# Performance work log

Hardware: AMD Instinct MI355X
Metric: run time of the kernel (lower is better)

Reference implementation:

```python
import jax, jax.numpy as jnp
import numpy as np

B, D, K = 131072, 64, 4096

def setup_inputs() -> dict:
    key = jax.random.key(0)
    k1, k2 = jax.random.split(key)
    z_e = jax.random.normal(k1, (B, D), dtype=jnp.float32)
    # nn.init.uniform_(-1/K, 1/K)
    codebook = jax.random.uniform(k2, (K, D), dtype=jnp.float32, minval=-1.0 / K, maxval=1.0 / K)
    return {"z_e": z_e, "codebook": codebook}

def reference(z_e, codebook):
    # squared-distance expansion: ||z||^2 + ||e||^2 - 2 z.e  -> (B, K)
    z2 = jnp.sum(z_e * z_e, axis=1, keepdims=True)          # (B, 1)
    e2 = jnp.sum(codebook * codebook, axis=1)[None, :]       # (1, K)
    ze = jnp.einsum('bd,kd->bk', z_e, codebook)              # (B, K)
    dist = z2 + e2 - 2.0 * ze
    codes = jnp.argmin(dist, axis=1)                         # (B,) int
    z_q = codebook[codes]                                    # (B, D) gather
    return (z_q, codes)
```

## Files before the change

### kernel.cpp

```cpp
#include <hip/hip_runtime.h>
#include <math.h>
#include <stdint.h>

#define Bn 131072
#define Dn 64
#define Kn 4096
#define TK 64
#define NKT (Kn / TK)
#define TPR 4
#define NRD (NKT / TPR)

typedef _Float16 f16x8 __attribute__((ext_vector_type(8)));
typedef float f32x4 __attribute__((ext_vector_type(4)));

__device__ __forceinline__ unsigned umn(unsigned a, unsigned b) { return a < b ? a : b; }
__device__ __forceinline__ unsigned umed3(unsigned a, unsigned b, unsigned c) {
  unsigned d;
  asm("v_med3_u32 %0, %1, %2, %3" : "=v"(d) : "v"(a), "v"(b), "v"(c));
  return d;
}

__device__ __forceinline__ void stage16(const void* g, void* l) {
  __builtin_amdgcn_global_load_lds((const __attribute__((address_space(1))) unsigned int*)g,
                                   (__attribute__((address_space(3))) unsigned int*)l,
                                   16, 0, 0);
}

__global__ __launch_bounds__(256) void cvt_cb(const float* __restrict__ cb,
                                              unsigned char* __restrict__ img) {
  int u = blockIdx.x * 256 + threadIdx.x;
  int g = u >> 3;
  int p = u & 7;
  int kt = g >> 6;
  int n = g & 63;
  const float4* s = (const float4*)(cb + (size_t)g * Dn + p * 8);
  float4 c0 = s[0], c1 = s[1];
  f16x8 h;
  h[0] = (_Float16)(c0.x * 4096.f); h[1] = (_Float16)(c0.y * 4096.f);
  h[2] = (_Float16)(c0.z * 4096.f); h[3] = (_Float16)(c0.w * 4096.f);
  h[4] = (_Float16)(c1.x * 4096.f); h[5] = (_Float16)(c1.y * 4096.f);
  h[6] = (_Float16)(c1.z * 4096.f); h[7] = (_Float16)(c1.w * 4096.f);
  *(f16x8*)(img + (size_t)kt * 8192 + n * 128 + ((p ^ (n & 7)) << 4)) = h;
}

template <int RB, int WB>
__device__ __forceinline__ void round_body(int rd, int tid,
                                           unsigned char* smem_,
                                           const unsigned char* b0,
                                           const unsigned char* b1,
                                           const unsigned char* wsrc,
                                           const f16x8 (&A)[4][2],
                                           unsigned (&k1)[4][4], unsigned (&k2)[4][4],
                                           unsigned (&tg)[4], const f32x4 c256) {
  asm volatile("s_waitcnt vmcnt(0)" ::: "memory");
  __builtin_amdgcn_s_barrier();
  __builtin_amdgcn_sched_barrier(0);
  if (rd + 1 < NRD) {
#pragma unroll
    for (int j = 0; j < TPR; ++j) {
      const unsigned char* gs = wsrc + ((size_t)(rd + 1) * TPR + j) * 8192;
      stage16(gs, smem_ + WB + j * 8192 + tid * 16);
      stage16(gs + 4096, smem_ + WB + j * 8192 + 4096 + tid * 16);
    }
  }
#pragma unroll
  for (int j = 0; j < TPR; ++j) {
#pragma unroll
    for (int t = 0; t < 4; ++t) {
      const f16x8 B0 = *(const f16x8*)(b0 + RB + j * 8192 + t * 2048);
      const f16x8 B1 = *(const f16x8*)(b1 + RB + j * 8192 + t * 2048);
      f32x4 a0 = __builtin_amdgcn_mfma_f32_16x16x32_f16(A[0][0], B0, c256, 0, 0, 0);
      f32x4 a1 = __builtin_amdgcn_mfma_f32_16x16x32_f16(A[1][0], B0, c256, 0, 0, 0);
      f32x4 a2 = __builtin_amdgcn_mfma_f32_16x16x32_f16(A[2][0], B0, c256, 0, 0, 0);
      f32x4 a3 = __builtin_amdgcn_mfma_f32_16x16x32_f16(A[3][0], B0, c256, 0, 0, 0);
      a0 = __builtin_amdgcn_mfma_f32_16x16x32_f16(A[0][1], B1, a0, 0, 0, 0);
      a1 = __builtin_amdgcn_mfma_f32_16x16x32_f16(A[1][1], B1, a1, 0, 0, 0);
      a2 = __builtin_amdgcn_mfma_f32_16x16x32_f16(A[2][1], B1, a2, 0, 0, 0);
      a3 = __builtin_amdgcn_mfma_f32_16x16x32_f16(A[3][1], B1, a3, 0, 0, 0);
#pragma unroll
      for (int r = 0; r < 4; ++r) {
        unsigned key0 = (__float_as_uint(a0[r]) & 0xFFFFFF00u) | tg[t];
        k2[0][r] = umed3(k1[0][r], k2[0][r], key0);
        k1[0][r] = umn(k1[0][r], key0);
        unsigned key1 = (__float_as_uint(a1[r]) & 0xFFFFFF00u) | tg[t];
        k2[1][r] = umed3(k1[1][r], k2[1][r], key1);
        k1[1][r] = umn(k1[1][r], key1);
        unsigned key2 = (__float_as_uint(a2[r]) & 0xFFFFFF00u) | tg[t];
        k2[2][r] = umed3(k1[2][r], k2[2][r], key2);
        k1[2][r] = umn(k1[2][r], key2);
        unsigned key3 = (__float_as_uint(a3[r]) & 0xFFFFFF00u) | tg[t];
        k2[3][r] = umed3(k1[3][r], k2[3][r], key3);
        k1[3][r] = umn(k1[3][r], key3);
      }
    }
#pragma unroll
    for (int t = 0; t < 4; ++t) tg[t] += 1;
  }
}

__global__ __launch_bounds__(256, 2) void vq_main(const float* __restrict__ z,
                                                  const float* __restrict__ cb,
                                                  const unsigned char* __restrict__ img,
                                                  float* __restrict__ out) {
  __shared__ __align__(16) unsigned char smem[66560];
  const int tid = threadIdx.x;
  const int lane = tid & 63;
  const int w = tid >> 6;
  const int q = lane >> 4;
  const int col = lane & 15;
  const int row0 = blockIdx.x * 256;

  const unsigned char* wsrc = img + tid * 16;
#pragma unroll
  for (int j = 0; j < TPR; ++j) {
    stage16(wsrc + (size_t)j * 8192, smem + j * 8192 + tid * 16);
    stage16(wsrc + (size_t)j * 8192 + 4096, smem + j * 8192 + 4096 + tid * 16);
  }

  f16x8 A[4][2];
#pragma unroll
  for (int i = 0; i < 4; ++i)
#pragma unroll
    for (int c = 0; c < 2; ++c) {
      const float* zp = z + (size_t)(row0 + w * 64 + i * 16 + col) * Dn + c * 32 + q * 8;
      float4 x0 = *(const float4*)zp;
      float4 x1 = *(const float4*)(zp + 4);
      f16x8 a;
      a[0] = (_Float16)(-2.f * x0.x); a[1] = (_Float16)(-2.f * x0.y);
      a[2] = (_Float16)(-2.f * x0.z); a[3] = (_Float16)(-2.f * x0.w);
      a[4] = (_Float16)(-2.f * x1.x); a[5] = (_Float16)(-2.f * x1.y);
      a[6] = (_Float16)(-2.f * x1.z); a[7] = (_Float16)(-2.f * x1.w);
      A[i][c] = a;
    }

  unsigned k1[4][4], k2[4][4];
#pragma unroll
  for (int i = 0; i < 4; ++i)
#pragma unroll
    for (int r = 0; r < 4; ++r) { k1[i][r] = 0xFFFFFFFFu; k2[i][r] = 0xFFFFFFFFu; }
  unsigned tg[4] = {0u << 6, 1u << 6, 2u << 6, 3u << 6};
  const f32x4 c256 = {256.f, 256.f, 256.f, 256.f};

  const int xu = (col & 7) << 4;
  const unsigned char* b0 = smem + col * 128 + ((q << 4) ^ xu);
  const unsigned char* b1 = smem + col * 128 + (((4 + q) << 4) ^ xu);

#pragma unroll 1
  for (int rp = 0; rp < NRD / 2; ++rp) {
    round_body<0, 32768>(2 * rp, tid, smem, b0, b1, wsrc, A, k1, k2, tg, c256);
    round_body<32768, 0>(2 * rp + 1, tid, smem, b0, b1, wsrc, A, k1, k2, tg, c256);
  }

  __syncthreads();
  unsigned* dmp = (unsigned*)smem;
#pragma unroll
  for (int i = 0; i < 4; ++i)
#pragma unroll
    for (int r = 0; r < 4; ++r) {
      int rb = w * 64 + i * 16 + q * 4 + r;
      dmp[rb * 33 + col * 2] = k1[i][r];
      dmp[rb * 33 + col * 2 + 1] = k2[i][r];
    }
  __syncthreads();

  {
    const int rl = tid;
    const unsigned* keys = dmp + rl * 33;
    unsigned mk = 0xFFFFFFFFu;
    for (int j = 0; j < 32; ++j) mk = umn(mk, keys[j]);
    const float lim = __uint_as_float(mk & 0xFFFFFF00u) + 0.5f;

    const float4* zr4 = (const float4*)(z + (size_t)(row0 + rl) * Dn);

    float r8[8];
#pragma unroll
    for (int g = 0; g < 2; ++g) {
      float4 v = zr4[g]; int j = g * 4;
      r8[j + 0] = __fmul_rn(v.x, v.x); r8[j + 1] = __fmul_rn(v.y, v.y);
      r8[j + 2] = __fmul_rn(v.z, v.z); r8[j + 3] = __fmul_rn(v.w, v.w);
    }
#pragma unroll
    for (int g = 2; g < 16; ++g) {
      float4 v = zr4[g]; int j = (g & 1) * 4;
      r8[j + 0] = __fadd_rn(r8[j + 0], __fmul_rn(v.x, v.x));
      r8[j + 1] = __fadd_rn(r8[j + 1], __fmul_rn(v.y, v.y));
      r8[j + 2] = __fadd_rn(r8[j + 2], __fmul_rn(v.z, v.z));
      r8[j + 3] = __fadd_rn(r8[j + 3], __fmul_rn(v.w, v.w));
    }
    float z2f = __fadd_rn(__fadd_rn(__fadd_rn(r8[0], r8[1]), __fadd_rn(r8[2], r8[3])),
                          __fadd_rn(__fadd_rn(r8[4], r8[5]), __fadd_rn(r8[6], r8[7])));

    float bq = INFINITY; int bc = Kn;
    for (int j = 0; j < 32; ++j) {
      unsigned key = keys[j];
      float sc = __uint_as_float(key & 0xFFFFFF00u);
      if (sc > lim) continue;
      int tag = (int)(key & 0xFFu);
      int code = (tag & 63) * 64 + (tag >> 6) * 16 + (j >> 1);
      const float4* cr = (const float4*)(cb + (size_t)code * Dn);
      double ze = 0.0;
      float e8[8];
#pragma unroll
      for (int g = 0; g < 16; ++g) {
        float4 ev = cr[g]; float4 zv = zr4[g];
        ze += (double)ev.x * (double)zv.x + (double)ev.y * (double)zv.y +
              (double)ev.z * (double)zv.z + (double)ev.w * (double)zv.w;
        int jj = (g & 1) * 4;
        if (g < 2) {
          e8[jj + 0] = __fmul_rn(ev.x, ev.x); e8[jj + 1] = __fmul_rn(ev.y, ev.y);
          e8[jj + 2] = __fmul_rn(ev.z, ev.z); e8[jj + 3] = __fmul_rn(ev.w, ev.w);
        } else {
          e8[jj + 0] = __fadd_rn(e8[jj + 0], __fmul_rn(ev.x, ev.x));
          e8[jj + 1] = __fadd_rn(e8[jj + 1], __fmul_rn(ev.y, ev.y));
          e8[jj + 2] = __fadd_rn(e8[jj + 2], __fmul_rn(ev.z, ev.z));
          e8[jj + 3] = __fadd_rn(e8[jj + 3], __fmul_rn(ev.w, ev.w));
        }
      }
      float e2f = __fadd_rn(__fadd_rn(__fadd_rn(e8[0], e8[1]), __fadd_rn(e8[2], e8[3])),
                            __fadd_rn(__fadd_rn(e8[4], e8[5]), __fadd_rn(e8[6], e8[7])));
      float zef = (float)ze;
      float t1 = __fadd_rn(z2f, e2f);
      float t2 = __fmul_rn(2.0f, zef);
      float qv = __fadd_rn(t1, -t2);
      if (qv < bq || (qv == bq && code < bc)) { bq = qv; bc = code; }
    }
    ((int*)(smem + 65536))[rl] = bc;
    out[(size_t)Bn * Dn + row0 + rl] = (float)bc;
  }
  __syncthreads();

  {
    const float4* cb4 = (const float4*)cb;
    float4* out4 = (float4*)out;
    const int* wc = (const int*)(smem + 65536);
#pragma unroll
    for (int i = 0; i < 16; ++i) {
      int t = i * 256 + tid;
      int r = t >> 4, c2 = t & 15;
      int wn = wc[r];
      out4[(size_t)(row0 + r) * 16 + c2] = cb4[(size_t)wn * 16 + c2];
    }
  }
}

extern "C" void kernel_launch(void* const* d_in, const int* in_sizes, int n_in,
                              void* d_out, int out_size, void* d_ws, size_t ws_size,
                              hipStream_t stream) {
  const float* z = (const float*)d_in[0];
  const float* cb = (const float*)d_in[1];
  float* out = (float*)d_out;
  unsigned char* img = (unsigned char*)d_ws;
  cvt_cb<<<128, 256, 0, stream>>>(cb, img);
  vq_main<<<Bn / 256, 256, 0, stream>>>(z, cb, img, out);
}
```

Before: 197.9 us.

## Split codebook across two wave groups per block, doubling threads to 512

Each block now runs 512 threads. Two groups of four waves each scan half of the codebook (tiles 0-31 and 32-63) for the same 256 rows, and each group stages only its own two tiles per round. The per-row candidate keys from both halves go into a wider shared dump, the exact rescoring is split over thread pairs, and the pair is merged with a shuffle. This is meant to raise wave-level parallelism and latency hiding per CU, at the cost of loading and converting the A operands twice and a larger final merge.

Result: slower. 219.3 us (+10.8%).

```diff
diff --git a/kernel.cpp b/kernel.cpp
--- a/kernel.cpp
+++ b/kernel.cpp
@@ -7,8 +7,7 @@
 #define Kn 4096
 #define TK 64
 #define NKT (Kn / TK)
-#define TPR 4
-#define NRD (NKT / TPR)
+#define NRD 16
 
 typedef _Float16 f16x8 __attribute__((ext_vector_type(8)));
 typedef float f32x4 __attribute__((ext_vector_type(4)));
@@ -56,15 +55,14 @@
   __builtin_amdgcn_s_barrier();
   __builtin_amdgcn_sched_barrier(0);
   if (rd + 1 < NRD) {
-#pragma unroll
-    for (int j = 0; j < TPR; ++j) {
-      const unsigned char* gs = wsrc + ((size_t)(rd + 1) * TPR + j) * 8192;
-      stage16(gs, smem_ + WB + j * 8192 + tid * 16);
-      stage16(gs + 4096, smem_ + WB + j * 8192 + 4096 + tid * 16);
-    }
-  }
-#pragma unroll
-  for (int j = 0; j < TPR; ++j) {
+    const size_t nt = 2 * (size_t)(rd + 1);
+    stage16(wsrc + nt * 8192, smem_ + WB + 0 * 8192 + tid * 16);
+    stage16(wsrc + (nt + 1) * 8192, smem_ + WB + 1 * 8192 + tid * 16);
+    stage16(wsrc + (nt + 32) * 8192, smem_ + WB + 2 * 8192 + tid * 16);
+    stage16(wsrc + (nt + 33) * 8192, smem_ + WB + 3 * 8192 + tid * 16);
+  }
+#pragma unroll
+  for (int j = 0; j < 2; ++j) {
 #pragma unroll
     for (int t = 0; t < 4; ++t) {
       const f16x8 B0 = *(const f16x8*)(b0 + RB + j * 8192 + t * 2048);
@@ -98,31 +96,32 @@
   }
 }
 
-__global__ __launch_bounds__(256, 2) void vq_main(const float* __restrict__ z,
+__global__ __launch_bounds__(512, 4) void vq_main(const float* __restrict__ z,
                                                   const float* __restrict__ cb,
                                                   const unsigned char* __restrict__ img,
                                                   float* __restrict__ out) {
-  __shared__ __align__(16) unsigned char smem[66560];
+  __shared__ __align__(16) unsigned char smem[67584];
   const int tid = threadIdx.x;
   const int lane = tid & 63;
   const int w = tid >> 6;
+  const int kh = w >> 2;
+  const int wq = w & 3;
   const int q = lane >> 4;
   const int col = lane & 15;
   const int row0 = blockIdx.x * 256;
 
   const unsigned char* wsrc = img + tid * 16;
-#pragma unroll
-  for (int j = 0; j < TPR; ++j) {
-    stage16(wsrc + (size_t)j * 8192, smem + j * 8192 + tid * 16);
-    stage16(wsrc + (size_t)j * 8192 + 4096, smem + j * 8192 + 4096 + tid * 16);
-  }
+  stage16(wsrc, smem + 0 * 8192 + tid * 16);
+  stage16(wsrc + 8192, smem + 1 * 8192 + tid * 16);
+  stage16(wsrc + (size_t)32 * 8192, smem + 2 * 8192 + tid * 16);
+  stage16(wsrc + (size_t)33 * 8192, smem + 3 * 8192 + tid * 16);
 
   f16x8 A[4][2];
 #pragma unroll
   for (int i = 0; i < 4; ++i)
 #pragma unroll
     for (int c = 0; c < 2; ++c) {
-      const float* zp = z + (size_t)(row0 + w * 64 + i * 16 + col) * Dn + c * 32 + q * 8;
+      const float* zp = z + (size_t)(row0 + wq * 64 + i * 16 + col) * Dn + c * 32 + q * 8;
       float4 x0 = *(const float4*)zp;
       float4 x1 = *(const float4*)(zp + 4);
       f16x8 a;
@@ -138,12 +137,14 @@
   for (int i = 0; i < 4; ++i)
 #pragma unroll
     for (int r = 0; r < 4; ++r) { k1[i][r] = 0xFFFFFFFFu; k2[i][r] = 0xFFFFFFFFu; }
-  unsigned tg[4] = {0u << 6, 1u << 6, 2u << 6, 3u << 6};
+  unsigned tg[4];
+#pragma unroll
+  for (int t = 0; t < 4; ++t) tg[t] = ((unsigned)t << 6) | ((unsigned)kh << 5);
   const f32x4 c256 = {256.f, 256.f, 256.f, 256.f};
 
   const int xu = (col & 7) << 4;
-  const unsigned char* b0 = smem + col * 128 + ((q << 4) ^ xu);
-  const unsigned char* b1 = smem + col * 128 + (((4 + q) << 4) ^ xu);
+  const unsigned char* b0 = smem + kh * 16384 + col * 128 + ((q << 4) ^ xu);
+  const unsigned char* b1 = smem + kh * 16384 + col * 128 + (((4 + q) << 4) ^ xu);
 
 #pragma unroll 1
   for (int rp = 0; rp < NRD / 2; ++rp) {
@@ -157,15 +158,17 @@
   for (int i = 0; i < 4; ++i)
 #pragma unroll
     for (int r = 0; r < 4; ++r) {
-      int rb = w * 64 + i * 16 + q * 4 + r;
-      dmp[rb * 33 + col * 2] = k1[i][r];
-      dmp[rb * 33 + col * 2 + 1] = k2[i][r];
+      int rb = wq * 64 + i * 16 + q * 4 + r;
+      int base = rb * 65 + kh * 32 + col * 2;
+      dmp[base] = k1[i][r];
+      dmp[base + 1] = k2[i][r];
     }
   __syncthreads();
 
   {
-    const int rl = tid;
-    const unsigned* keys = dmp + rl * 33;
+    const int rl = tid >> 1;
+    const int hp = tid & 1;
+    const unsigned* keys = dmp + rl * 65 + hp * 32;
     unsigned mk = 0xFFFFFFFFu;
     for (int j = 0; j < 32; ++j) mk = umn(mk, keys[j]);
     const float lim = __uint_as_float(mk & 0xFFFFFF00u) + 0.5f;
@@ -224,18 +227,23 @@
       float qv = __fadd_rn(t1, -t2);
       if (qv < bq || (qv == bq && code < bc)) { bq = qv; bc = code; }
     }
-    ((int*)(smem + 65536))[rl] = bc;
-    out[(size_t)Bn * Dn + row0 + rl] = (float)bc;
+    float obq = __shfl_xor(bq, 1);
+    int obc = __shfl_xor(bc, 1);
+    if (obq < bq || (obq == bq && obc < bc)) { bq = obq; bc = obc; }
+    if (hp == 0) {
+      ((int*)(smem + 66560))[rl] = bc;
+      out[(size_t)Bn * Dn + row0 + rl] = (float)bc;
+    }
   }
   __syncthreads();
 
   {
     const float4* cb4 = (const float4*)cb;
     float4* out4 = (float4*)out;
-    const int* wc = (const int*)(smem + 65536);
-#pragma unroll
-    for (int i = 0; i < 16; ++i) {
-      int t = i * 256 + tid;
+    const int* wc = (const int*)(smem + 66560);
+#pragma unroll
+    for (int i = 0; i < 8; ++i) {
+      int t = i * 512 + tid;
       int r = t >> 4, c2 = t & 15;
       int wn = wc[r];
       out4[(size_t)(row0 + r) * 16 + c2] = cb4[(size_t)wn * 16 + c2];
@@ -251,5 +259,5 @@
   float* out = (float*)d_out;
   unsigned char* img = (unsigned char*)d_ws;
   cvt_cb<<<128, 256, 0, stream>>>(cb, img);
-  vq_main<<<Bn / 256, 256, 0, stream>>>(z, cb, img, out);
-}
+  vq_main<<<Bn / 256, 512, 0, stream>>>(z, cb, img, out);
+}
```
